# Kernel tuning notes

Measured on AMD Instinct MI355X. Metric: run time of the kernel, lower is better.

## Reference

```python
import jax, jax.numpy as jnp
import numpy as np

H = 128          # image height (raster_settings.image_size)
W = 128          # image width
K = 8            # points per pixel kept in the z-buffer
CHUNK = 256      # point chunk size for streaming top-k merge
RADIUS = 0.02    # NDC splat radius
BIG = 1e10       # sentinel depth for empty / out-of-radius
EPS = 1e-6       # homogeneous-divide eps (transform_points eps)


def setup_inputs() -> dict:
    key = jax.random.key(0)
    kxy, kz = jax.random.split(key)
    B, N = 4, 8192
    # points inside a simple view frustum: z in [1,3], xy within +-0.5*z
    z = jax.random.uniform(kz, (B, N, 1), dtype=jnp.float32, minval=1.0, maxval=3.0)
    xy = jax.random.uniform(kxy, (B, N, 2), dtype=jnp.float32, minval=-1.0, maxval=1.0) * z * 0.5
    points = jnp.concatenate([xy, z], axis=-1)
    # world-to-view: identity (points already generated in view space)
    world_to_view = jnp.eye(4, dtype=jnp.float32)
    # simple perspective projection composed with ndc transform (row-vector convention):
    # q = [f*x, f*y, z, z]; after divide -> (f*x/z, f*y/z, 1); z later replaced by view z
    f = 2.0
    proj_to_ndc = jnp.array([[f, 0., 0., 0.],
                             [0., f, 0., 0.],
                             [0., 0., 1., 1.],
                             [0., 0., 0., 0.]], dtype=jnp.float32)
    return {"points": points, "world_to_view": world_to_view, "proj_to_ndc": proj_to_ndc}


def _transform(points, world_to_view, proj_to_ndc):
    # pytorch3d row-vector homogeneous transform_points with eps-safe divide
    ph = jnp.concatenate([points, jnp.ones_like(points[..., :1])], axis=-1)  # (B,N,4)
    pv = ph @ world_to_view
    view_z = pv[..., 2]
    q = pv @ proj_to_ndc
    w = q[..., 3:4]
    sgn = jnp.where(w >= 0, 1.0, -1.0)
    ndc = q[..., :3] / (sgn * jnp.maximum(jnp.abs(w), EPS))
    # pts_ndc[..., 2] = pts_view[..., 2]
    return ndc.at[..., 2].set(view_z)


def _rasterize(pts_ndc):
    # per-pixel z-buffer of the K nearest (smallest view-z) points whose NDC
    # xy distance^2 to the pixel center is <= radius^2, streamed over point chunks
    B, N, _ = pts_ndc.shape
    px = 1.0 - (2.0 * jnp.arange(W, dtype=jnp.float32) + 1.0) / W  # NDC x of pixel centers
    py = 1.0 - (2.0 * jnp.arange(H, dtype=jnp.float32) + 1.0) / H  # NDC y of pixel centers
    r2 = RADIUS * RADIUS
    n_chunks = N // CHUNK
    pts_c = pts_ndc.reshape(B, n_chunks, CHUNK, 3).transpose(1, 0, 2, 3)  # (S,B,C,3)
    base = (jnp.arange(n_chunks) * CHUNK).astype(jnp.int32)
    z0 = jnp.full((B, H, W, K), BIG, dtype=jnp.float32)
    i0 = jnp.full((B, H, W, K), -1, dtype=jnp.int32)
    d0 = jnp.zeros((B, H, W, K), dtype=jnp.float32)

    def body(carry, inp):
        zb, ib, db = carry
        pc, b0 = inp
        x, y, z = pc[..., 0], pc[..., 1], pc[..., 2]                 # (B,C)
        dx = x[:, None, None, :] - px[None, None, :, None]           # (B,1,W,C)
        dy = y[:, None, None, :] - py[None, :, None, None]           # (B,H,1,C)
        d2 = dx * dx + dy * dy                                        # (B,H,W,C)
        inside = (d2 <= r2) & (z[:, None, None, :] > 0)
        zc = jnp.where(inside, z[:, None, None, :], BIG)
        z_all = jnp.concatenate([zb, zc], axis=-1)                    # (B,H,W,K+C)
        d_all = jnp.concatenate([db, d2], axis=-1)
        neg_z, sel = jax.lax.top_k(-z_all, K)                         # K smallest z
        z_new = -neg_z
        d_new = jnp.take_along_axis(d_all, sel, axis=-1)
        i_old = jnp.take_along_axis(ib, jnp.minimum(sel, K - 1), axis=-1)
        i_new = jnp.where(sel < K, i_old, b0 + sel - K)               # global point ids
        return (z_new, i_new, d_new), None

    (zb, ib, db), _ = jax.lax.scan(body, (z0, i0, d0), (pts_c, base))
    valid = zb < BIG * 0.5
    zbuf = jnp.where(valid, zb, -1.0)
    idx = jnp.where(valid, ib, -1)
    dists2 = jnp.where(valid, db, -1.0)
    return idx, zbuf, dists2


def reference(points, world_to_view, proj_to_ndc):
    pts_ndc = _transform(points, world_to_view, proj_to_ndc)
    idx, zbuf, dists2 = _rasterize(pts_ndc)
    # PointFragments(idx, zbuf, zbuf_idx, dists)
    return idx, zbuf, idx, dists2
```

## Files before the change

### kernel.cpp

```cpp
#include <hip/hip_runtime.h>
#include <cstdint>

#define HD __device__ __forceinline__

constexpr int B = 4, N = 8192, H = 128, W = 128, K = 8;
constexpr float BIGF = 1e10f;
constexpr int TOTPIX = B * H * W;
constexpr int CAPP = 32;

HD bool keyless(float z1, int i1, float z2, int i2) {
    return (z1 < z2) || ((z1 == z2) && (i1 < i2));
}

HD void insert_topk(float nz, int ni, float nd,
                    float (&zk)[K], int (&ik)[K], float (&dk)[K]) {
    bool lt[K];
#pragma unroll
    for (int j = 0; j < K; ++j) lt[j] = keyless(nz, ni, zk[j], ik[j]);
#pragma unroll
    for (int j = K - 1; j >= 1; --j) {
        if (lt[j]) {
            if (lt[j - 1]) { zk[j] = zk[j - 1]; ik[j] = ik[j - 1]; dk[j] = dk[j - 1]; }
            else           { zk[j] = nz;        ik[j] = ni;        dk[j] = nd; }
        }
    }
    if (lt[0]) { zk[0] = nz; ik[0] = ni; dk[0] = nd; }
}

HD void transform_point(const float* __restrict__ w2v, const float* __restrict__ p2n,
                        float x, float y, float z,
                        float& xn, float& yn, float& zn) {
    float pv[4];
#pragma unroll
    for (int j = 0; j < 4; ++j)
        pv[j] = x * w2v[0 * 4 + j] + y * w2v[1 * 4 + j] +
                z * w2v[2 * 4 + j] + 1.0f * w2v[3 * 4 + j];
    float viewz = pv[2];
    float q[4];
#pragma unroll
    for (int j = 0; j < 4; ++j)
        q[j] = pv[0] * p2n[0 * 4 + j] + pv[1] * p2n[1 * 4 + j] +
               pv[2] * p2n[2 * 4 + j] + pv[3] * p2n[3 * 4 + j];
    float wq = q[3];
    float sgn = (wq >= 0.0f) ? 1.0f : -1.0f;
    float denom = sgn * fmaxf(fabsf(wq), 1e-6f);
    xn = q[0] / denom;
    yn = q[1] / denom;
    zn = viewz;
}

HD void write_out(float* __restrict__ out, int pix,
                  const float (&zk)[K], const int (&ik)[K], const float (&dk)[K]) {
    const size_t S = (size_t)TOTPIX * K;
    size_t off = (size_t)pix * K;
    float fi[K], fz[K], fd[K];
#pragma unroll
    for (int j = 0; j < K; ++j) {
        bool valid = zk[j] < 0.5f * BIGF;
        fi[j] = valid ? (float)ik[j] : -1.0f;
        fz[j] = valid ? zk[j] : -1.0f;
        fd[j] = valid ? dk[j] : -1.0f;
    }
    float4* o0 = reinterpret_cast<float4*>(out + off);
    float4* o1 = reinterpret_cast<float4*>(out + S + off);
    float4* o2 = reinterpret_cast<float4*>(out + 2 * S + off);
    float4* o3 = reinterpret_cast<float4*>(out + 3 * S + off);
    o0[0] = make_float4(fi[0], fi[1], fi[2], fi[3]);
    o0[1] = make_float4(fi[4], fi[5], fi[6], fi[7]);
    o1[0] = make_float4(fz[0], fz[1], fz[2], fz[3]);
    o1[1] = make_float4(fz[4], fz[5], fz[6], fz[7]);
    o2[0] = make_float4(fi[0], fi[1], fi[2], fi[3]);
    o2[1] = make_float4(fi[4], fi[5], fi[6], fi[7]);
    o3[0] = make_float4(fd[0], fd[1], fd[2], fd[3]);
    o3[1] = make_float4(fd[4], fd[5], fd[6], fd[7]);
}

__global__ __launch_bounds__(256) void zero_cnt_kernel(int4* __restrict__ cnt4) {
    int i = blockIdx.x * 256 + threadIdx.x;
    cnt4[i] = make_int4(0, 0, 0, 0);
}

__global__ __launch_bounds__(128) void bin_pixels_kernel(
    const float* __restrict__ points, const float* __restrict__ w2v,
    const float* __restrict__ p2n, int* __restrict__ cnt,
    float4* __restrict__ entries) {
    int gid = blockIdx.x * 128 + threadIdx.x;
    int b = gid >> 13;
    int n = gid & (N - 1);
    float x = points[(size_t)gid * 3 + 0];
    float y = points[(size_t)gid * 3 + 1];
    float z = points[(size_t)gid * 3 + 2];
    float xn, yn, zn;
    transform_point(w2v, p2n, x, y, z, xn, yn, zn);
    if (!(zn > 0.0f)) return;

    const float rb = 0.0201f;
    const float r2 = (float)(0.02 * 0.02);
    int wmin = (int)ceilf(((1.0f - xn) - rb) * 64.0f - 0.5f);
    int wmax = (int)floorf(((1.0f - xn) + rb) * 64.0f - 0.5f);
    int hmin = (int)ceilf(((1.0f - yn) - rb) * 64.0f - 0.5f);
    int hmax = (int)floorf(((1.0f - yn) + rb) * 64.0f - 0.5f);
    wmin = max(wmin, 0); wmax = min(wmax, W - 1);
    hmin = max(hmin, 0); hmax = min(hmax, H - 1);

    for (int h = hmin; h <= hmax; ++h) {
        float py = 1.0f - (2.0f * (float)h + 1.0f) / 128.0f;
        float dy = yn - py;
        float dy2 = __fmul_rn(dy, dy);
        for (int w = wmin; w <= wmax; ++w) {
            float px = 1.0f - (2.0f * (float)w + 1.0f) / 128.0f;
            float dx = xn - px;
            float d2 = __fadd_rn(__fmul_rn(dx, dx), dy2);
            if (d2 <= r2) {
                int pix = (b << 14) + (h << 7) + w;
                int pos = atomicAdd(&cnt[pix], 1);
                if (pos < CAPP)
                    entries[(size_t)pos * TOTPIX + pix] =
                        make_float4(zn, d2, __int_as_float(n), 0.0f);
            }
        }
    }
}

__global__ __launch_bounds__(256) void select_kernel(
    const int* __restrict__ cnt, const float4* __restrict__ entries,
    float* __restrict__ out) {
    int pix = blockIdx.x * 256 + threadIdx.x;
    int c = cnt[pix];
    if (c > CAPP) c = CAPP;

    float zk[K]; int ik[K]; float dk[K];
#pragma unroll
    for (int j = 0; j < K; ++j) { zk[j] = BIGF; ik[j] = 0x7fffffff; dk[j] = 0.0f; }

    for (int j = 0; j < c; ++j) {
        float4 e = entries[(size_t)j * TOTPIX + pix];
        int pi = __float_as_int(e.z);
        if (keyless(e.x, pi, zk[K - 1], ik[K - 1]))
            insert_topk(e.x, pi, e.y, zk, ik, dk);
    }
    write_out(out, pix, zk, ik, dk);
}

HD void process_candidate(float4 p, float px, float py, float r2,
                          float (&zk)[K], int (&ik)[K], float (&dk)[K]) {
    float dx = p.x - px, dy = p.y - py;
    float d2 = __fadd_rn(__fmul_rn(dx, dx), __fmul_rn(dy, dy));
    int pi = __float_as_int(p.w);
    if ((d2 <= r2) && (p.z > 0.0f) && keyless(p.z, pi, zk[K - 1], ik[K - 1]))
        insert_topk(p.z, pi, d2, zk, ik, dk);
}

__global__ __launch_bounds__(256) void brute_kernel(
    const float* __restrict__ points, const float* __restrict__ w2v,
    const float* __restrict__ p2n, float* __restrict__ out) {
    int gid = blockIdx.x * 256 + threadIdx.x;
    int b = gid >> 14;
    int rem = gid & 16383;
    int h = rem >> 7, w = rem & 127;
    float px = 1.0f - (2.0f * (float)w + 1.0f) / 128.0f;
    float py = 1.0f - (2.0f * (float)h + 1.0f) / 128.0f;
    const float r2 = (float)(0.02 * 0.02);

    __shared__ float4 sh[256];

    float zk[K]; int ik[K]; float dk[K];
#pragma unroll
    for (int j = 0; j < K; ++j) { zk[j] = BIGF; ik[j] = 0x7fffffff; dk[j] = 0.0f; }

    for (int c = 0; c < N; c += 256) {
        __syncthreads();
        int n = c + threadIdx.x;
        float x = points[((size_t)b * N + n) * 3 + 0];
        float y = points[((size_t)b * N + n) * 3 + 1];
        float z = points[((size_t)b * N + n) * 3 + 2];
        float xn, yn, zn;
        transform_point(w2v, p2n, x, y, z, xn, yn, zn);
        sh[threadIdx.x] = make_float4(xn, yn, zn, __int_as_float(n));
        __syncthreads();
        for (int e = 0; e < 256; ++e)
            process_candidate(sh[e], px, py, r2, zk, ik, dk);
    }
    write_out(out, gid, zk, ik, dk);
}

extern "C" void kernel_launch(void* const* d_in, const int* in_sizes, int n_in,
                              void* d_out, int out_size, void* d_ws, size_t ws_size,
                              hipStream_t stream) {
    const float* points = (const float*)d_in[0];
    const float* w2v    = (const float*)d_in[1];
    const float* p2n    = (const float*)d_in[2];
    float* out = (float*)d_out;

    const size_t cnt_bytes = (size_t)TOTPIX * sizeof(int);
    const size_t ent_off   = 1 << 20;
    const size_t need = ent_off + (size_t)CAPP * TOTPIX * sizeof(float4);

    if (ws_size >= need) {
        int* cnt = (int*)d_ws;
        float4* entries = (float4*)((char*)d_ws + ent_off);
        zero_cnt_kernel<<<TOTPIX / (256 * 4), 256, 0, stream>>>((int4*)cnt);
        bin_pixels_kernel<<<(B * N) / 128, 128, 0, stream>>>(points, w2v, p2n, cnt, entries);
        select_kernel<<<TOTPIX / 256, 256, 0, stream>>>(cnt, entries, out);
        (void)cnt_bytes;
    } else {
        brute_kernel<<<(B * H * W) / 256, 256, 0, stream>>>(points, w2v, p2n, out);
    }
}
```

Baseline: 29.02 us.

## Fuse zero, bin and select into one cooperative kernel with grid syncs

New measurement: 82.93 us. 2.86x slower.

```diff
diff --git a/kernel.cpp b/kernel.cpp
--- a/kernel.cpp
+++ b/kernel.cpp
@@ -1,5 +1,8 @@
 #include <hip/hip_runtime.h>
+#include <hip/hip_cooperative_groups.h>
 #include <cstdint>
+
+namespace cg = cooperative_groups;
 
 #define HD __device__ __forceinline__
 
@@ -7,6 +10,8 @@
 constexpr float BIGF = 1e10f;
 constexpr int TOTPIX = B * H * W;
 constexpr int CAPP = 32;
+constexpr int NBLK = 256;
+constexpr int NTHR = 256;
 
 HD bool keyless(float z1, int i1, float z2, int i2) {
     return (z1 < z2) || ((z1 == z2) && (i1 < i2));
@@ -71,75 +76,78 @@
     o1[1] = make_float4(fz[4], fz[5], fz[6], fz[7]);
     o2[0] = make_float4(fi[0], fi[1], fi[2], fi[3]);
     o2[1] = make_float4(fi[4], fi[5], fi[6], fi[7]);
-    o3[0] = make_float4(fd[0], fd[1], fd[2], fd[3]);
+    o3[0] = make_float4(fd[0], fd[1], fd[2], fd[7 - 7 + 3]);
     o3[1] = make_float4(fd[4], fd[5], fd[6], fd[7]);
 }
 
-__global__ __launch_bounds__(256) void zero_cnt_kernel(int4* __restrict__ cnt4) {
-    int i = blockIdx.x * 256 + threadIdx.x;
-    cnt4[i] = make_int4(0, 0, 0, 0);
-}
-
-__global__ __launch_bounds__(128) void bin_pixels_kernel(
+__global__ __launch_bounds__(NTHR) void fused_coop_kernel(
     const float* __restrict__ points, const float* __restrict__ w2v,
     const float* __restrict__ p2n, int* __restrict__ cnt,
-    float4* __restrict__ entries) {
-    int gid = blockIdx.x * 128 + threadIdx.x;
-    int b = gid >> 13;
-    int n = gid & (N - 1);
-    float x = points[(size_t)gid * 3 + 0];
-    float y = points[(size_t)gid * 3 + 1];
-    float z = points[(size_t)gid * 3 + 2];
-    float xn, yn, zn;
-    transform_point(w2v, p2n, x, y, z, xn, yn, zn);
-    if (!(zn > 0.0f)) return;
-
-    const float rb = 0.0201f;
-    const float r2 = (float)(0.02 * 0.02);
-    int wmin = (int)ceilf(((1.0f - xn) - rb) * 64.0f - 0.5f);
-    int wmax = (int)floorf(((1.0f - xn) + rb) * 64.0f - 0.5f);
-    int hmin = (int)ceilf(((1.0f - yn) - rb) * 64.0f - 0.5f);
-    int hmax = (int)floorf(((1.0f - yn) + rb) * 64.0f - 0.5f);
-    wmin = max(wmin, 0); wmax = min(wmax, W - 1);
-    hmin = max(hmin, 0); hmax = min(hmax, H - 1);
-
-    for (int h = hmin; h <= hmax; ++h) {
-        float py = 1.0f - (2.0f * (float)h + 1.0f) / 128.0f;
-        float dy = yn - py;
-        float dy2 = __fmul_rn(dy, dy);
-        for (int w = wmin; w <= wmax; ++w) {
-            float px = 1.0f - (2.0f * (float)w + 1.0f) / 128.0f;
-            float dx = xn - px;
-            float d2 = __fadd_rn(__fmul_rn(dx, dx), dy2);
-            if (d2 <= r2) {
-                int pix = (b << 14) + (h << 7) + w;
-                int pos = atomicAdd(&cnt[pix], 1);
-                if (pos < CAPP)
-                    entries[(size_t)pos * TOTPIX + pix] =
-                        make_float4(zn, d2, __int_as_float(n), 0.0f);
+    float4* __restrict__ entries, float* __restrict__ out) {
+    cg::grid_group grid = cg::this_grid();
+    int tid = blockIdx.x * NTHR + threadIdx.x;
+
+    cnt[tid] = 0;
+    grid.sync();
+
+    {
+        int p = tid >> 1;
+        int par = tid & 1;
+        int b = p >> 13;
+        int n = p & (N - 1);
+        float x = points[(size_t)p * 3 + 0];
+        float y = points[(size_t)p * 3 + 1];
+        float z = points[(size_t)p * 3 + 2];
+        float xn, yn, zn;
+        transform_point(w2v, p2n, x, y, z, xn, yn, zn);
+        if (zn > 0.0f) {
+            const float rb = 0.0201f;
+            const float r2 = (float)(0.02 * 0.02);
+            int wmin = (int)ceilf(((1.0f - xn) - rb) * 64.0f - 0.5f);
+            int wmax = (int)floorf(((1.0f - xn) + rb) * 64.0f - 0.5f);
+            int hmin = (int)ceilf(((1.0f - yn) - rb) * 64.0f - 0.5f);
+            int hmax = (int)floorf(((1.0f - yn) + rb) * 64.0f - 0.5f);
+            wmin = max(wmin, 0); wmax = min(wmax, W - 1);
+            hmin = max(hmin, 0); hmax = min(hmax, H - 1);
+
+            for (int h = hmin + par; h <= hmax; h += 2) {
+                float py = 1.0f - (2.0f * (float)h + 1.0f) / 128.0f;
+                float dy = yn - py;
+                float dy2 = __fmul_rn(dy, dy);
+                for (int w = wmin; w <= wmax; ++w) {
+                    float px = 1.0f - (2.0f * (float)w + 1.0f) / 128.0f;
+                    float dx = xn - px;
+                    float d2 = __fadd_rn(__fmul_rn(dx, dx), dy2);
+                    if (d2 <= r2) {
+                        int pix = (b << 14) + (h << 7) + w;
+                        int pos = atomicAdd(&cnt[pix], 1);
+                        if (pos < CAPP)
+                            entries[(size_t)pos * TOTPIX + pix] =
+                                make_float4(zn, d2, __int_as_float(n), 0.0f);
+                    }
+                }
             }
         }
     }
-}
-
-__global__ __launch_bounds__(256) void select_kernel(
-    const int* __restrict__ cnt, const float4* __restrict__ entries,
-    float* __restrict__ out) {
-    int pix = blockIdx.x * 256 + threadIdx.x;
-    int c = cnt[pix];
-    if (c > CAPP) c = CAPP;
-
-    float zk[K]; int ik[K]; float dk[K];
-#pragma unroll
-    for (int j = 0; j < K; ++j) { zk[j] = BIGF; ik[j] = 0x7fffffff; dk[j] = 0.0f; }
-
-    for (int j = 0; j < c; ++j) {
-        float4 e = entries[(size_t)j * TOTPIX + pix];
-        int pi = __float_as_int(e.z);
-        if (keyless(e.x, pi, zk[K - 1], ik[K - 1]))
-            insert_topk(e.x, pi, e.y, zk, ik, dk);
-    }
-    write_out(out, pix, zk, ik, dk);
+    grid.sync();
+
+    {
+        int pix = tid;
+        int c = cnt[pix];
+        if (c > CAPP) c = CAPP;
+
+        float zk[K]; int ik[K]; float dk[K];
+#pragma unroll
+        for (int j = 0; j < K; ++j) { zk[j] = BIGF; ik[j] = 0x7fffffff; dk[j] = 0.0f; }
+
+        for (int j = 0; j < c; ++j) {
+            float4 e = entries[(size_t)j * TOTPIX + pix];
+            int pi = __float_as_int(e.z);
+            if (keyless(e.x, pi, zk[K - 1], ik[K - 1]))
+                insert_topk(e.x, pi, e.y, zk, ik, dk);
+        }
+        write_out(out, pix, zk, ik, dk);
+    }
 }
 
 HD void process_candidate(float4 p, float px, float py, float r2,
@@ -156,10 +164,8 @@
     const float* __restrict__ p2n, float* __restrict__ out) {
     int gid = blockIdx.x * 256 + threadIdx.x;
     int b = gid >> 14;
-    int rem = gid & 16383;
-    int h = rem >> 7, w = rem & 127;
-    float px = 1.0f - (2.0f * (float)w + 1.0f) / 128.0f;
-    float py = 1.0f - (2.0f * (float)h + 1.0f) / 128.0f;
+    float px = 1.0f - (2.0f * (float)(gid & 127) + 1.0f) / 128.0f;
+    float py = 1.0f - (2.0f * (float)((gid >> 7) & 127) + 1.0f) / 128.0f;
     const float r2 = (float)(0.02 * 0.02);
 
     __shared__ float4 sh[256];
@@ -192,17 +198,16 @@
     const float* p2n    = (const float*)d_in[2];
     float* out = (float*)d_out;
 
-    const size_t cnt_bytes = (size_t)TOTPIX * sizeof(int);
-    const size_t ent_off   = 1 << 20;
+    const size_t ent_off = 1 << 20;
     const size_t need = ent_off + (size_t)CAPP * TOTPIX * sizeof(float4);
 
     if (ws_size >= need) {
         int* cnt = (int*)d_ws;
         float4* entries = (float4*)((char*)d_ws + ent_off);
-        zero_cnt_kernel<<<TOTPIX / (256 * 4), 256, 0, stream>>>((int4*)cnt);
-        bin_pixels_kernel<<<(B * N) / 128, 128, 0, stream>>>(points, w2v, p2n, cnt, entries);
-        select_kernel<<<TOTPIX / 256, 256, 0, stream>>>(cnt, entries, out);
-        (void)cnt_bytes;
+        void* args[] = { (void*)&points, (void*)&w2v, (void*)&p2n,
+                         (void*)&cnt, (void*)&entries, (void*)&out };
+        hipLaunchCooperativeKernel((const void*)fused_coop_kernel,
+                                   dim3(NBLK), dim3(NTHR), args, 0, stream);
     } else {
         brute_kernel<<<(B * H * W) / 256, 256, 0, stream>>>(points, w2v, p2n, out);
     }
```

## Fuse count zeroing with point transform staging, split binning into own kernel

Applied to the files above, without the earlier changes.

New measurement: 29.09 us. About the same (+0.3%).

```diff
diff --git a/kernel.cpp b/kernel.cpp
--- a/kernel.cpp
+++ b/kernel.cpp
@@ -25,28 +25,6 @@
         }
     }
     if (lt[0]) { zk[0] = nz; ik[0] = ni; dk[0] = nd; }
-}
-
-HD void transform_point(const float* __restrict__ w2v, const float* __restrict__ p2n,
-                        float x, float y, float z,
-                        float& xn, float& yn, float& zn) {
-    float pv[4];
-#pragma unroll
-    for (int j = 0; j < 4; ++j)
-        pv[j] = x * w2v[0 * 4 + j] + y * w2v[1 * 4 + j] +
-                z * w2v[2 * 4 + j] + 1.0f * w2v[3 * 4 + j];
-    float viewz = pv[2];
-    float q[4];
-#pragma unroll
-    for (int j = 0; j < 4; ++j)
-        q[j] = pv[0] * p2n[0 * 4 + j] + pv[1] * p2n[1 * 4 + j] +
-               pv[2] * p2n[2 * 4 + j] + pv[3] * p2n[3 * 4 + j];
-    float wq = q[3];
-    float sgn = (wq >= 0.0f) ? 1.0f : -1.0f;
-    float denom = sgn * fmaxf(fabsf(wq), 1e-6f);
-    xn = q[0] / denom;
-    yn = q[1] / denom;
-    zn = viewz;
 }
 
 HD void write_out(float* __restrict__ out, int pix,
@@ -75,48 +53,74 @@
     o3[1] = make_float4(fd[4], fd[5], fd[6], fd[7]);
 }
 
-__global__ __launch_bounds__(256) void zero_cnt_kernel(int4* __restrict__ cnt4) {
-    int i = blockIdx.x * 256 + threadIdx.x;
-    cnt4[i] = make_int4(0, 0, 0, 0);
-}
-
-__global__ __launch_bounds__(128) void bin_pixels_kernel(
+__global__ __launch_bounds__(256) void stage_zero_kernel(
     const float* __restrict__ points, const float* __restrict__ w2v,
-    const float* __restrict__ p2n, int* __restrict__ cnt,
-    float4* __restrict__ entries) {
-    int gid = blockIdx.x * 128 + threadIdx.x;
-    int b = gid >> 13;
-    int n = gid & (N - 1);
+    const float* __restrict__ p2n, float4* __restrict__ staged,
+    int4* __restrict__ cnt4) {
+    __shared__ float lc[16];
+    int tid = threadIdx.x;
+    if (tid < 16) {
+        int r = tid & 3, sel = tid >> 2;
+        float v;
+        if (sel < 3) {
+            int j = (sel == 0) ? 0 : (sel == 1) ? 1 : 3;
+            v = w2v[r * 4 + 0] * p2n[0 * 4 + j] + w2v[r * 4 + 1] * p2n[1 * 4 + j] +
+                w2v[r * 4 + 2] * p2n[2 * 4 + j] + w2v[r * 4 + 3] * p2n[3 * 4 + j];
+        } else {
+            v = w2v[r * 4 + 2];
+        }
+        lc[tid] = v;
+    }
+    __syncthreads();
+
+    int gid = blockIdx.x * 256 + tid;
+    if (gid < TOTPIX / 4) cnt4[gid] = make_int4(0, 0, 0, 0);
+
     float x = points[(size_t)gid * 3 + 0];
     float y = points[(size_t)gid * 3 + 1];
     float z = points[(size_t)gid * 3 + 2];
-    float xn, yn, zn;
-    transform_point(w2v, p2n, x, y, z, xn, yn, zn);
-    if (!(zn > 0.0f)) return;
+    float q0 = x * lc[0]  + y * lc[1]  + z * lc[2]  + lc[3];
+    float q1 = x * lc[4]  + y * lc[5]  + z * lc[6]  + lc[7];
+    float q3 = x * lc[8]  + y * lc[9]  + z * lc[10] + lc[11];
+    float zn = x * lc[12] + y * lc[13] + z * lc[14] + lc[15];
+    float sgn = (q3 >= 0.0f) ? 1.0f : -1.0f;
+    float den = sgn * fmaxf(fabsf(q3), 1e-6f);
+    float xn = q0 / den, yn = q1 / den;
+    if (!(zn > 0.0f)) xn = 1e30f;
+    staged[gid] = make_float4(xn, yn, zn, __int_as_float(gid & (N - 1)));
+}
+
+__global__ __launch_bounds__(256) void bin_kernel(
+    const float4* __restrict__ staged, int* __restrict__ cnt,
+    float4* __restrict__ entries) {
+    int gid = blockIdx.x * 256 + threadIdx.x;
+    float4 e = staged[gid];
+    if (fabsf(e.x) > 1.013f || fabsf(e.y) > 1.013f) return;
+    int b = gid >> 13;
 
     const float rb = 0.0201f;
     const float r2 = (float)(0.02 * 0.02);
-    int wmin = (int)ceilf(((1.0f - xn) - rb) * 64.0f - 0.5f);
-    int wmax = (int)floorf(((1.0f - xn) + rb) * 64.0f - 0.5f);
-    int hmin = (int)ceilf(((1.0f - yn) - rb) * 64.0f - 0.5f);
-    int hmax = (int)floorf(((1.0f - yn) + rb) * 64.0f - 0.5f);
+    int wmin = (int)ceilf(((1.0f - e.x) - rb) * 64.0f - 0.5f);
+    int wmax = (int)floorf(((1.0f - e.x) + rb) * 64.0f - 0.5f);
+    int hmin = (int)ceilf(((1.0f - e.y) - rb) * 64.0f - 0.5f);
+    int hmax = (int)floorf(((1.0f - e.y) + rb) * 64.0f - 0.5f);
     wmin = max(wmin, 0); wmax = min(wmax, W - 1);
     hmin = max(hmin, 0); hmax = min(hmax, H - 1);
 
     for (int h = hmin; h <= hmax; ++h) {
         float py = 1.0f - (2.0f * (float)h + 1.0f) / 128.0f;
-        float dy = yn - py;
+        float dy = e.y - py;
         float dy2 = __fmul_rn(dy, dy);
         for (int w = wmin; w <= wmax; ++w) {
             float px = 1.0f - (2.0f * (float)w + 1.0f) / 128.0f;
-            float dx = xn - px;
+            float dx = e.x - px;
             float d2 = __fadd_rn(__fmul_rn(dx, dx), dy2);
             if (d2 <= r2) {
                 int pix = (b << 14) + (h << 7) + w;
                 int pos = atomicAdd(&cnt[pix], 1);
                 if (pos < CAPP)
                     entries[(size_t)pos * TOTPIX + pix] =
-                        make_float4(zn, d2, __int_as_float(n), 0.0f);
+                        make_float4(e.z, d2, e.w, 0.0f);
             }
         }
     }
@@ -142,13 +146,21 @@
     write_out(out, pix, zk, ik, dk);
 }
 
-HD void process_candidate(float4 p, float px, float py, float r2,
-                          float (&zk)[K], int (&ik)[K], float (&dk)[K]) {
-    float dx = p.x - px, dy = p.y - py;
-    float d2 = __fadd_rn(__fmul_rn(dx, dx), __fmul_rn(dy, dy));
-    int pi = __float_as_int(p.w);
-    if ((d2 <= r2) && (p.z > 0.0f) && keyless(p.z, pi, zk[K - 1], ik[K - 1]))
-        insert_topk(p.z, pi, d2, zk, ik, dk);
+HD void transform_point_full(const float* __restrict__ w2v, const float* __restrict__ p2n,
+                             float x, float y, float z,
+                             float& xn, float& yn, float& zn) {
+    float pv[4];
+#pragma unroll
+    for (int j = 0; j < 4; ++j)
+        pv[j] = x * w2v[0 * 4 + j] + y * w2v[1 * 4 + j] +
+                z * w2v[2 * 4 + j] + 1.0f * w2v[3 * 4 + j];
+    float viewz = pv[2];
+    float q0 = pv[0] * p2n[0] + pv[1] * p2n[4] + pv[2] * p2n[8]  + pv[3] * p2n[12];
+    float q1 = pv[0] * p2n[1] + pv[1] * p2n[5] + pv[2] * p2n[9]  + pv[3] * p2n[13];
+    float q3 = pv[0] * p2n[3] + pv[1] * p2n[7] + pv[2] * p2n[11] + pv[3] * p2n[15];
+    float sgn = (q3 >= 0.0f) ? 1.0f : -1.0f;
+    float den = sgn * fmaxf(fabsf(q3), 1e-6f);
+    xn = q0 / den; yn = q1 / den; zn = viewz;
 }
 
 __global__ __launch_bounds__(256) void brute_kernel(
@@ -156,10 +168,8 @@
     const float* __restrict__ p2n, float* __restrict__ out) {
     int gid = blockIdx.x * 256 + threadIdx.x;
     int b = gid >> 14;
-    int rem = gid & 16383;
-    int h = rem >> 7, w = rem & 127;
-    float px = 1.0f - (2.0f * (float)w + 1.0f) / 128.0f;
-    float py = 1.0f - (2.0f * (float)h + 1.0f) / 128.0f;
+    float px = 1.0f - (2.0f * (float)(gid & 127) + 1.0f) / 128.0f;
+    float py = 1.0f - (2.0f * (float)((gid >> 7) & 127) + 1.0f) / 128.0f;
     const float r2 = (float)(0.02 * 0.02);
 
     __shared__ float4 sh[256];
@@ -175,11 +185,17 @@
         float y = points[((size_t)b * N + n) * 3 + 1];
         float z = points[((size_t)b * N + n) * 3 + 2];
         float xn, yn, zn;
-        transform_point(w2v, p2n, x, y, z, xn, yn, zn);
+        transform_point_full(w2v, p2n, x, y, z, xn, yn, zn);
         sh[threadIdx.x] = make_float4(xn, yn, zn, __int_as_float(n));
         __syncthreads();
-        for (int e = 0; e < 256; ++e)
-            process_candidate(sh[e], px, py, r2, zk, ik, dk);
+        for (int e = 0; e < 256; ++e) {
+            float4 pe = sh[e];
+            float dx = pe.x - px, dy = pe.y - py;
+            float d2 = __fadd_rn(__fmul_rn(dx, dx), __fmul_rn(dy, dy));
+            int pi = __float_as_int(pe.w);
+            if ((d2 <= r2) && (pe.z > 0.0f) && keyless(pe.z, pi, zk[K - 1], ik[K - 1]))
+                insert_topk(pe.z, pi, d2, zk, ik, dk);
+        }
     }
     write_out(out, gid, zk, ik, dk);
 }
@@ -192,17 +208,18 @@
     const float* p2n    = (const float*)d_in[2];
     float* out = (float*)d_out;
 
-    const size_t cnt_bytes = (size_t)TOTPIX * sizeof(int);
-    const size_t ent_off   = 1 << 20;
+    const size_t staged_off = 256 << 10;
+    const size_t ent_off    = 1 << 20;
     const size_t need = ent_off + (size_t)CAPP * TOTPIX * sizeof(float4);
 
     if (ws_size >= need) {
-        int* cnt = (int*)d_ws;
+        int* cnt        = (int*)d_ws;
+        float4* staged  = (float4*)((char*)d_ws + staged_off);
         float4* entries = (float4*)((char*)d_ws + ent_off);
-        zero_cnt_kernel<<<TOTPIX / (256 * 4), 256, 0, stream>>>((int4*)cnt);
-        bin_pixels_kernel<<<(B * N) / 128, 128, 0, stream>>>(points, w2v, p2n, cnt, entries);
+        stage_zero_kernel<<<(B * N) / 256, 256, 0, stream>>>(points, w2v, p2n,
+                                                             staged, (int4*)cnt);
+        bin_kernel<<<(B * N) / 256, 256, 0, stream>>>(staged, cnt, entries);
         select_kernel<<<TOTPIX / 256, 256, 0, stream>>>(cnt, entries, out);
-        (void)cnt_bytes;
     } else {
         brute_kernel<<<(B * H * W) / 256, 256, 0, stream>>>(points, w2v, p2n, out);
     }
```
